# Kernel tuning notes

Hardware: AMD Instinct MI355X
Metric: run time of the kernel (lower is better)

Reference implementation:

```python
import jax, jax.numpy as jnp
import numpy as np

B, S, D, H = 1, 2048, 1024, 16
HD = D // H
S_SLOPE = 10.0      # soft_thres_layer s
C_MASK = -10000.0   # soft_thres_layer c == masked_bias
ALPHA = 0.0         # config.threshold
W_STD = 0.02        # GPT2 init std for weights


def setup_inputs() -> dict:
    key = jax.random.key(0)
    k1, k2, k3 = jax.random.split(key, 3)
    return {
        "hidden_states": jax.random.normal(k1, (B, S, D), dtype=jnp.float32),
        "c_attn_w": jax.random.normal(k2, (D, 3 * D), dtype=jnp.float32) * W_STD,
        "c_attn_b": jnp.zeros((3 * D,), dtype=jnp.float32),
        "c_proj_w": jax.random.normal(k3, (D, D), dtype=jnp.float32) * W_STD,
        "c_proj_b": jnp.zeros((D,), dtype=jnp.float32),
    }


def reference(hidden_states, c_attn_w, c_attn_b, c_proj_w, c_proj_b):
    # Conv1D: x @ w + b (GPT2 convention: weight is [in, out])
    qkv = hidden_states @ c_attn_w + c_attn_b            # [B,S,3D]
    q, k, v = jnp.split(qkv, 3, axis=-1)

    def split_heads(x):
        return x.reshape(B, S, H, HD).transpose(0, 2, 1, 3)  # [B,H,S,hd]

    q, k, v = split_heads(q), split_heads(k), split_heads(v)

    # prun path: NO 1/sqrt(d) scaling (skipped when self.prun is True)
    w = jnp.einsum("bhqd,bhkd->bhqk", q, k)              # [B,H,S,S]

    causal = jnp.tril(jnp.ones((S, S), dtype=bool))[None, None]
    w = jnp.where(causal, w, C_MASK)

    # soft-threshold pruning: smoothly pushes scores below alpha toward c=-10000
    w = C_MASK + (w - C_MASK) * jax.nn.sigmoid(S_SLOPE * (w - ALPHA))

    a = jax.nn.softmax(w, axis=-1)                        # attn_dropout = identity (eval)
    out = jnp.einsum("bhqk,bhkd->bhqd", a, v)             # [B,H,S,hd]
    out = out.transpose(0, 2, 1, 3).reshape(B, S, D)      # merge heads
    return out @ c_proj_w + c_proj_b                      # resid_dropout = identity
```

## Files before the change

kernel.cpp:

```cpp
#include <hip/hip_runtime.h>


#define S_LEN 2048
#define DM    1024
#define NH    16
#define HD    64
#define SLOPE 10.0f
#define CMASK -10000.0f
#define SP    2080

typedef short s16x4 __attribute__((ext_vector_type(4)));
typedef short s16x8 __attribute__((ext_vector_type(8)));
typedef float f32x4 __attribute__((ext_vector_type(4)));

#define MFMA16(a,b,c) __builtin_amdgcn_mfma_f32_16x16x32_bf16(a,b,c,0,0,0)
#define GLDS16(g,l) __builtin_amdgcn_global_load_lds( \
    (const __attribute__((address_space(1))) void*)(g), \
    (__attribute__((address_space(3))) void*)(l), 16, 0, 0)

__device__ __forceinline__ short f2bf(float f){
    unsigned u = __float_as_uint(f);
    u += 0x7fffu + ((u >> 16) & 1u);
    return (short)(u >> 16);
}
__device__ __forceinline__ float bf2f(short x){
    return __uint_as_float(((unsigned)(unsigned short)x) << 16);
}
struct bfpair { short hi, lo; };
__device__ __forceinline__ bfpair split_bf(float x){
    bfpair r; r.hi = f2bf(x);
    r.lo = f2bf(x - bf2f(r.hi));
    return r;
}

__device__ __forceinline__ float softthr(float sv){
    float E = __expf(-SLOPE*sv);
    float w = sv - __fdividef((sv - CMASK)*E, 1.f + E);
    return (sv > -1.5f) ? w : CMASK;
}

template<int ROWS, int THREADS>
__device__ __forceinline__ void stage_tile(const short* gbase, int rstride,
                                           short* lds, int tid){
#pragma unroll
    for (int it = 0; it < ROWS*8/THREADS; ++it){
        int s = it*THREADS + tid;
        int row = s >> 3, grp = s & 7;
        const short* src = gbase + (size_t)row*rstride + ((grp ^ (row & 7)) << 3);
        GLDS16(src, lds + (size_t)s*8);
    }
}
__device__ __forceinline__ s16x8 frag(const short* lds, int row, int kg){
    return *(const s16x8*)&lds[row*64 + ((kg ^ (row & 7)) << 3)];
}

__global__ __launch_bounds__(256)
void prep(const float* __restrict__ hs, const float* __restrict__ wqkv,
          const float* __restrict__ wprj, short* __restrict__ Ahl,
          short* __restrict__ WqT, short* __restrict__ WkvT,
          short* __restrict__ WpT)
{
    __shared__ float t[64][65];
    const int bx = blockIdx.x, tid = threadIdx.x;

    if (bx < 2048){
        int i = bx*256 + tid;
        int elem = i*4, row = elem >> 10, col = elem & 1023;
        float4 v = *(const float4*)&hs[(size_t)elem];
        bfpair a = split_bf(v.x), b = split_bf(v.y), c = split_bf(v.z), d = split_bf(v.w);
        s16x4 hv, lv;
        hv.x = a.hi; hv.y = b.hi; hv.z = c.hi; hv.w = d.hi;
        lv.x = a.lo; lv.y = b.lo; lv.z = c.lo; lv.w = d.lo;
        *(s16x4*)&Ahl[(size_t)row*2048 + col] = hv;
        *(s16x4*)&Ahl[(size_t)row*2048 + 1024 + col] = lv;
        return;
    }

    const float* W; int N, u;
    if (bx < 2816){ u = bx - 2048; W = wqkv; N = 3072; }
    else          { u = bx - 2816; W = wprj; N = 1024; }
    const int ntiles = N >> 6;
    const int tn = (u % ntiles)*64, tk = (u / ntiles)*64;

#pragma unroll
    for (int it = 0; it < 4; ++it){
        int idx = tid + it*256;
        int r = idx >> 4, c4 = (idx & 15)*4;
        float4 v = *(const float4*)&W[(size_t)(tk + r)*N + tn + c4];
        t[r][c4] = v.x; t[r][c4+1] = v.y; t[r][c4+2] = v.z; t[r][c4+3] = v.w;
    }
    __syncthreads();
#pragma unroll
    for (int it = 0; it < 4; ++it){
        int idx = tid + it*256;
        int n = idx >> 4, c4 = (idx & 15)*4;
        s16x4 hv, lv;
#pragma unroll
        for (int j = 0; j < 4; ++j){
            bfpair p = split_bf(t[c4+j][n]);
            hv[j] = p.hi; lv[j] = p.lo;
        }
        if (bx >= 2816){
            *(s16x4*)&WpT[(size_t)(tn + n)*1024 + tk + c4] = hv;
        } else if (tn < 1024){
            *(s16x4*)&WqT[(size_t)(tn + n)*2048 + tk + c4] = hv;
            *(s16x4*)&WqT[(size_t)(tn + n)*2048 + 1024 + tk + c4] = lv;
        } else {
            *(s16x4*)&WkvT[(size_t)(tn + n - 1024)*1024 + tk + c4] = hv;
        }
    }
}

__global__ __launch_bounds__(256)
void gemm_qkv(const short* __restrict__ Ahl, const short* __restrict__ WqT,
              const short* __restrict__ WkvT, const float* __restrict__ bias,
              short* __restrict__ QHh, short* __restrict__ QHl,
              short* __restrict__ KH,  short* __restrict__ Vb)
{
    __shared__ __align__(16) short Ah_s[128*64];
    __shared__ __align__(16) short Bh_s[128*64];

    const int tid = threadIdx.x, lane = tid & 63, wid = tid >> 6;
    const int lr = lane & 15, lg = lane >> 4;
    const int brow = blockIdx.y*128;
    const int xs = blockIdx.x % 3, xi = blockIdx.x / 3;
    const int bcol = xs*1024 + xi*128;
    const bool isQ = (xs == 0);
    const int KTOT = isQ ? 3072 : 1024;
    const short* Bbase = isQ ? (WqT + (size_t)bcol*2048)
                             : (WkvT + (size_t)(bcol - 1024)*1024);
    const int bstride = isQ ? 2048 : 1024;
    const int wm = (wid >> 1)*64, wn = (wid & 1)*64;

    f32x4 acc[4][4];
#pragma unroll
    for (int m = 0; m < 4; ++m)
#pragma unroll
        for (int n = 0; n < 4; ++n) acc[m][n] = (f32x4){0.f,0.f,0.f,0.f};

    for (int k0 = 0; k0 < KTOT; k0 += 64){
        int acol  = (k0 < 2048) ? k0 : k0 - 2048;
        int bcolk = (isQ && k0 >= 1024) ? k0 - 1024 : k0;
        stage_tile<128,256>(Ahl + (size_t)brow*2048 + acol, 2048, Ah_s, tid);
        stage_tile<128,256>(Bbase + bcolk, bstride, Bh_s, tid);
        __syncthreads();
#pragma unroll
        for (int kc = 0; kc < 2; ++kc){
            s16x8 ah[4], bh[4];
#pragma unroll
            for (int m = 0; m < 4; ++m)
                ah[m] = frag(Ah_s, wm + m*16 + lr, kc*4 + lg);
#pragma unroll
            for (int n = 0; n < 4; ++n)
                bh[n] = frag(Bh_s, wn + n*16 + lr, kc*4 + lg);
#pragma unroll
            for (int m = 0; m < 4; ++m)
#pragma unroll
                for (int n = 0; n < 4; ++n)
                    acc[m][n] = MFMA16(ah[m], bh[n], acc[m][n]);
        }
        __syncthreads();
    }

#pragma unroll
    for (int m = 0; m < 4; ++m)
#pragma unroll
        for (int n = 0; n < 4; ++n){
            int row  = brow + wm + m*16 + lg*4;
            int gcol = bcol + wn + n*16 + lr;
            float bv = bias[gcol];
            int col1 = gcol & 1023;
            int h0 = col1 >> 6, d = col1 & 63;
#pragma unroll
            for (int v = 0; v < 4; ++v){
                float val = acc[m][n][v] + bv;
                if (xs == 0){
                    bfpair p = split_bf(val);
                    size_t o = ((size_t)h0*S_LEN + row + v)*HD + d;
                    QHh[o] = p.hi; QHl[o] = p.lo;
                } else if (xs == 1){
                    KH[((size_t)h0*S_LEN + row + v)*HD + d] = f2bf(val);
                } else {
                    Vb[(size_t)(row + v)*DM + col1] = f2bf(val);
                }
            }
        }
}

__global__ __launch_bounds__(256)
void gemm_proj(const short* __restrict__ Ahg, const short* __restrict__ Bhg,
               const float* __restrict__ bias, float* __restrict__ C)
{
    __shared__ __align__(16) short Ah_s[128*64];
    __shared__ __align__(16) short Bh_s[128*64];

    const int tid = threadIdx.x, lane = tid & 63, wid = tid >> 6;
    const int lr = lane & 15, lg = lane >> 4;
    const int brow = blockIdx.y*128, bcol = blockIdx.x*128;
    const int wm = (wid >> 1)*64, wn = (wid & 1)*64;

    f32x4 acc[4][4];
#pragma unroll
    for (int m = 0; m < 4; ++m)
#pragma unroll
        for (int n = 0; n < 4; ++n) acc[m][n] = (f32x4){0.f,0.f,0.f,0.f};

    for (int k0 = 0; k0 < DM; k0 += 64){
        stage_tile<128,256>(Ahg + (size_t)brow*DM + k0, DM, Ah_s, tid);
        stage_tile<128,256>(Bhg + (size_t)bcol*DM + k0, DM, Bh_s, tid);
        __syncthreads();
#pragma unroll
        for (int kc = 0; kc < 2; ++kc){
            s16x8 ah[4], bh[4];
#pragma unroll
            for (int m = 0; m < 4; ++m)
                ah[m] = frag(Ah_s, wm + m*16 + lr, kc*4 + lg);
#pragma unroll
            for (int n = 0; n < 4; ++n)
                bh[n] = frag(Bh_s, wn + n*16 + lr, kc*4 + lg);
#pragma unroll
            for (int m = 0; m < 4; ++m)
#pragma unroll
                for (int n = 0; n < 4; ++n)
                    acc[m][n] = MFMA16(ah[m], bh[n], acc[m][n]);
        }
        __syncthreads();
    }

#pragma unroll
    for (int m = 0; m < 4; ++m)
#pragma unroll
        for (int n = 0; n < 4; ++n){
            int row  = brow + wm + m*16 + lg*4;
            int gcol = bcol + wn + n*16 + lr;
            float bv = bias[gcol];
#pragma unroll
            for (int v = 0; v < 4; ++v)
                C[(size_t)(row + v)*DM + gcol] = acc[m][n][v] + bv;
        }
}

__global__ __launch_bounds__(256)
void vtrans(const short* __restrict__ Vb, short* __restrict__ Vt,
            float* __restrict__ PB)
{
    __shared__ short t[64][66];
    const int tid = threadIdx.x;
    const int h = blockIdx.x, b = blockIdx.y;
    const int td = h*64, ts = b*64;
#pragma unroll
    for (int it = 0; it < 4; ++it){
        int idx = tid + it*256;
        int r = idx >> 4, c4 = (idx & 15)*4;
        s16x4 v = *(const s16x4*)&Vb[(size_t)(ts + r)*DM + td + c4];
        t[r][c4] = v.x; t[r][c4+1] = v.y; t[r][c4+2] = v.z; t[r][c4+3] = v.w;
    }
    __syncthreads();
#pragma unroll
    for (int it = 0; it < 4; ++it){
        int idx = tid + it*256;
        int n = idx >> 4, c4 = (idx & 15)*4;
        s16x4 o;
#pragma unroll
        for (int j = 0; j < 4; ++j) o[j] = t[c4+j][n];
        *(s16x4*)&Vt[(size_t)(td + n)*SP + ts + c4] = o;
    }
    if (tid < 64){
        float s = 0.f;
#pragma unroll 8
        for (int r = 0; r < 64; ++r) s += bf2f(t[r][tid]);
        PB[((size_t)h*32 + b)*64 + tid] = s;
    }
}

__global__ __launch_bounds__(64)
void sv_suffix(const float* __restrict__ PB, float* __restrict__ SSV)
{
    int h = blockIdx.x, d = threadIdx.x;
    float s = 0.f;
    SSV[((size_t)h*33 + 32)*64 + d] = 0.f;
    for (int b = 31; b >= 0; --b){
        s += PB[((size_t)h*32 + b)*64 + d];
        SSV[((size_t)h*33 + b)*64 + d] = s;
    }
}

__global__ __launch_bounds__(256)
void attn_fwd(const short* __restrict__ QHh, const short* __restrict__ QHl,
              const short* __restrict__ KH, const short* __restrict__ Vt,
              short* __restrict__ acc0, short* __restrict__ acc1,
              short* __restrict__ acc2, float* __restrict__ ML)
{
    __shared__ __align__(16) short kh_s[64*64];
    __shared__ __align__(16) short vt_s[64*64];
    __shared__ __align__(16) short Ps[4][16*72];

    const int j = blockIdx.x;
    const int h = (j & 7) + 8*((j >> 3) & 1);
    const int t = j >> 4;
    int qst, c;
    if (t < 8)      { qst = t; c = 0; }
    else if (t < 24){ int u = t - 8;  qst = 8  + (u >> 1); c = u & 1; }
    else if (t < 48){ int u = t - 24; qst = 16 + u/3;      c = u - (u/3)*3; }
    else            { int u = t - 48; qst = 24 + (u >> 2); c = u & 3; }
    const int kv0 = c*8;
    const int kv1 = min(kv0 + 8, qst + 1);

    const int tid = threadIdx.x, lane = tid & 63, wid = tid >> 6;
    const int lr = lane & 15, lg = lane >> 4;
    const int qrow = qst*64 + wid*16 + lg*4;

    const short* qbh = QHh + ((size_t)h*S_LEN + qst*64 + wid*16)*HD;
    const short* qbl = QHl + ((size_t)h*S_LEN + qst*64 + wid*16)*HD;
    s16x8 aqh[2], aql[2];
#pragma unroll
    for (int kc = 0; kc < 2; ++kc){
        aqh[kc] = *(const s16x8*)&qbh[lr*HD + kc*32 + lg*8];
        aql[kc] = *(const s16x8*)&qbl[lr*HD + kc*32 + lg*8];
    }

    float m_run[4], l_run[4];
    f32x4 acc_o[4];
#pragma unroll
    for (int v = 0; v < 4; ++v){ m_run[v] = -1e30f; l_run[v] = 0.f; }
#pragma unroll
    for (int n = 0; n < 4; ++n) acc_o[n] = (f32x4){0.f,0.f,0.f,0.f};

    for (int kvb = kv0; kvb < kv1; ++kvb){
        __syncthreads();
        stage_tile<64,256>(KH + ((size_t)h*S_LEN + kvb*64)*HD, HD, kh_s, tid);
        stage_tile<64,256>(Vt + (size_t)(h*HD)*SP + kvb*64, SP, vt_s, tid);
        __syncthreads();

        f32x4 sc[4];
#pragma unroll
        for (int n = 0; n < 4; ++n) sc[n] = (f32x4){0.f,0.f,0.f,0.f};
#pragma unroll
        for (int kc = 0; kc < 2; ++kc)
#pragma unroll
            for (int n = 0; n < 4; ++n){
                s16x8 bkh = frag(kh_s, n*16 + lr, kc*4 + lg);
                sc[n] = MFMA16(aqh[kc], bkh, sc[n]);
                sc[n] = MFMA16(aql[kc], bkh, sc[n]);
            }

        float p[4][4], tmax[4];
#pragma unroll
        for (int v = 0; v < 4; ++v) tmax[v] = -1e30f;
        if (kvb == qst){
#pragma unroll
            for (int n = 0; n < 4; ++n){
                int key = kvb*64 + n*16 + lr;
#pragma unroll
                for (int v = 0; v < 4; ++v){
                    float w = (key > qrow + v) ? CMASK : softthr(sc[n][v]);
                    p[n][v] = w;
                    tmax[v] = fmaxf(tmax[v], w);
                }
            }
        } else {
#pragma unroll
            for (int n = 0; n < 4; ++n)
#pragma unroll
                for (int v = 0; v < 4; ++v){
                    float w = softthr(sc[n][v]);
                    p[n][v] = w;
                    tmax[v] = fmaxf(tmax[v], w);
                }
        }
#pragma unroll
        for (int v = 0; v < 4; ++v)
#pragma unroll
            for (int msk = 1; msk < 16; msk <<= 1)
                tmax[v] = fmaxf(tmax[v], __shfl_xor(tmax[v], msk, 64));

        float scale[4], rsum[4];
#pragma unroll
        for (int v = 0; v < 4; ++v){
            float mn = fmaxf(m_run[v], tmax[v]);
            scale[v] = __expf(m_run[v] - mn);
            m_run[v] = mn;
            rsum[v] = 0.f;
        }
#pragma unroll
        for (int n = 0; n < 4; ++n)
#pragma unroll
            for (int v = 0; v < 4; ++v){
                float e = __expf(p[n][v] - m_run[v]);
                p[n][v] = e;
                rsum[v] += e;
            }
#pragma unroll
        for (int v = 0; v < 4; ++v){
#pragma unroll
            for (int msk = 1; msk < 16; msk <<= 1)
                rsum[v] += __shfl_xor(rsum[v], msk, 64);
            l_run[v] = l_run[v]*scale[v] + rsum[v];
        }
#pragma unroll
        for (int n = 0; n < 4; ++n)
#pragma unroll
            for (int v = 0; v < 4; ++v) acc_o[n][v] *= scale[v];

#pragma unroll
        for (int n = 0; n < 4; ++n)
#pragma unroll
            for (int v = 0; v < 4; ++v)
                Ps[wid][(lg*4 + v)*72 + 16*n + lr] = f2bf(p[n][v]);
        asm volatile("s_waitcnt lgkmcnt(0)" ::: "memory");

        s16x8 pa0 = *(const s16x8*)&Ps[wid][lr*72 + lg*8];
        s16x8 pa1 = *(const s16x8*)&Ps[wid][lr*72 + 32 + lg*8];
#pragma unroll
        for (int n = 0; n < 4; ++n){
            s16x8 bv0 = frag(vt_s, 16*n + lr, lg);
            s16x8 bv1 = frag(vt_s, 16*n + lr, 4 + lg);
            acc_o[n] = MFMA16(pa0, bv0, acc_o[n]);
            acc_o[n] = MFMA16(pa1, bv1, acc_o[n]);
        }
    }

    short* ab = (j < 512)  ? acc0 + (size_t)j*4096
              : (j < 1024) ? acc1 + (size_t)(j-512)*4096
                           : acc2 + (size_t)(j-1024)*4096;
#pragma unroll
    for (int n = 0; n < 4; ++n)
#pragma unroll
        for (int v = 0; v < 4; ++v)
            ab[(wid*16 + lg*4 + v)*64 + 16*n + lr] = f2bf(acc_o[n][v]);
    if (lr == 0){
#pragma unroll
        for (int v = 0; v < 4; ++v){
            ML[((size_t)j*64 + wid*16 + lg*4 + v)*2 + 0] = m_run[v];
            ML[((size_t)j*64 + wid*16 + lg*4 + v)*2 + 1] = l_run[v];
        }
    }
}

__global__ __launch_bounds__(256)
void attn_merge(const short* __restrict__ acc0, const short* __restrict__ acc1,
                const short* __restrict__ acc2, const float* __restrict__ ML,
                const float* __restrict__ SSV, short* __restrict__ O)
{
    const int b = blockIdx.x;
    const int h = b & 15, qst = b >> 4;
    const int d = threadIdx.x & 63, rg = threadIdx.x >> 6;
    const int C = (qst + 8) >> 3;
    const int tbase = (qst < 8)  ? qst
                    : (qst < 16) ? 8  + 2*(qst - 8)
                    : (qst < 24) ? 24 + 3*(qst - 16)
                                 : 48 + 4*(qst - 24);
    const float F = (float)(S_LEN - 64*(qst + 1));
    const float svd = SSV[((size_t)h*33 + (qst + 1))*64 + d];

    for (int i = 0; i < 16; ++i){
        int r = rg + 4*i;
        float M = -1e30f;
        for (int c = 0; c < C; ++c){
            int job = (tbase + c)*16 + h;
            M = fmaxf(M, ML[((size_t)job*64 + r)*2]);
        }
        float num = 0.f, den = 0.f;
        for (int c = 0; c < C; ++c){
            int job = (tbase + c)*16 + h;
            float m = ML[((size_t)job*64 + r)*2];
            float l = ML[((size_t)job*64 + r)*2 + 1];
            const short* ab = (job < 512)  ? acc0 + (size_t)job*4096
                            : (job < 1024) ? acc1 + (size_t)(job-512)*4096
                                           : acc2 + (size_t)(job-1024)*4096;
            float e = __expf(m - M);
            num += e * bf2f(ab[r*64 + d]);
            den += e * l;
        }
        float et = __expf(CMASK - M);
        num += et * svd;
        den += et * F;
        O[(size_t)(qst*64 + r)*DM + h*64 + d] = f2bf(num * __fdividef(1.f, den));
    }
}

extern "C" void kernel_launch(void* const* d_in, const int* in_sizes, int n_in,
                              void* d_out, int out_size, void* d_ws, size_t ws_size,
                              hipStream_t stream)
{
    (void)in_sizes; (void)n_in; (void)out_size; (void)ws_size;
    const float* hs   = (const float*)d_in[0];
    const float* wqkv = (const float*)d_in[1];
    const float* bqkv = (const float*)d_in[2];
    const float* wprj = (const float*)d_in[3];
    const float* bprj = (const float*)d_in[4];

    char* p = (char*)d_ws;
    short* Ahl  = (short*)(p + (0ull  << 20));
    short* WqT  = (short*)(p + (8ull  << 20));
    short* WkvT = (short*)(p + (12ull << 20));
    short* WpT  = (short*)(p + (16ull << 20));
    short* QHh  = (short*)(p + (18ull << 20));
    short* QHl  = (short*)(p + (22ull << 20));
    short* KH   = (short*)(p + (26ull << 20));
    short* Vbg  = (short*)(p + (30ull << 20));
    short* VT   = (short*)(p + (34ull << 20));
    float* PB   = (float*)(p + (38ull << 20) + (256ull << 10));
    float* SSV  = (float*)(p + (38ull << 20) + (512ull << 10));
    short* O    = Ahl;
    short* accA = (short*)(p + (4ull  << 20));
    short* accB = (short*)(p + (8ull  << 20));
    short* accC = (short*)(p + (12ull << 20));
    float* ML   = (float*)(p + (14ull << 20));

    prep<<<3072, 256, 0, stream>>>(hs, wqkv, wprj, Ahl, WqT, WkvT, WpT);

    gemm_qkv<<<dim3(24, 16), 256, 0, stream>>>(
        Ahl, WqT, WkvT, bqkv, QHh, QHl, KH, Vbg);

    vtrans<<<dim3(NH, S_LEN/64), 256, 0, stream>>>(Vbg, VT, PB);
    sv_suffix<<<NH, 64, 0, stream>>>(PB, SSV);

    attn_fwd<<<1280, 256, 0, stream>>>(QHh, QHl, KH, VT, accA, accB, accC, ML);
    attn_merge<<<512, 256, 0, stream>>>(accA, accB, accC, ML, SSV, O);

    gemm_proj<<<dim3(8, 16), 256, 0, stream>>>(O, WpT, bprj, (float*)d_out);
}
```

Baseline: 195.6 us.

## Restructure QKV GEMM into fused hi/lo k-loop with 32-wide tiles; inline sigmoid

After: 176.2 us. 1.11x faster.

```diff
diff --git a/kernel.cpp b/kernel.cpp
--- a/kernel.cpp
+++ b/kernel.cpp
@@ -33,12 +33,6 @@
     return r;
 }
 
-__device__ __forceinline__ float softthr(float sv){
-    float E = __expf(-SLOPE*sv);
-    float w = sv - __fdividef((sv - CMASK)*E, 1.f + E);
-    return (sv > -1.5f) ? w : CMASK;
-}
-
 template<int ROWS, int THREADS>
 __device__ __forceinline__ void stage_tile(const short* gbase, int rstride,
                                            short* lds, int tid){
@@ -52,6 +46,21 @@
 }
 __device__ __forceinline__ s16x8 frag(const short* lds, int row, int kg){
     return *(const s16x8*)&lds[row*64 + ((kg ^ (row & 7)) << 3)];
+}
+
+template<int ROWS, int THREADS>
+__device__ __forceinline__ void stage32(const short* gbase, int rstride,
+                                        short* lds, int tid){
+#pragma unroll
+    for (int it = 0; it < ROWS*4/THREADS; ++it){
+        int s = it*THREADS + tid;
+        int row = s >> 2, grp = s & 3;
+        const short* src = gbase + (size_t)row*rstride + ((grp ^ ((row >> 1) & 3)) << 3);
+        GLDS16(src, lds + (size_t)s*8);
+    }
+}
+__device__ __forceinline__ s16x8 frag32(const short* lds, int row, int kg){
+    return *(const s16x8*)&lds[row*32 + ((kg ^ ((row >> 1) & 3)) << 3)];
 }
 
 __global__ __launch_bounds__(256)
@@ -117,8 +126,7 @@
               short* __restrict__ QHh, short* __restrict__ QHl,
               short* __restrict__ KH,  short* __restrict__ Vb)
 {
-    __shared__ __align__(16) short Ah_s[128*64];
-    __shared__ __align__(16) short Bh_s[128*64];
+    __shared__ __align__(16) short LDS[4][128*32];
 
     const int tid = threadIdx.x, lane = tid & 63, wid = tid >> 6;
     const int lr = lane & 15, lg = lane >> 4;
@@ -126,10 +134,10 @@
     const int xs = blockIdx.x % 3, xi = blockIdx.x / 3;
     const int bcol = xs*1024 + xi*128;
     const bool isQ = (xs == 0);
-    const int KTOT = isQ ? 3072 : 1024;
-    const short* Bbase = isQ ? (WqT + (size_t)bcol*2048)
+    const short* Abase = Ahl + (size_t)brow*2048;
+    const short* Bbase = isQ ? (WqT + (size_t)(xi*128)*2048)
                              : (WkvT + (size_t)(bcol - 1024)*1024);
-    const int bstride = isQ ? 2048 : 1024;
+    const int bstr = isQ ? 2048 : 1024;
     const int wm = (wid >> 1)*64, wn = (wid & 1)*64;
 
     f32x4 acc[4][4];
@@ -138,27 +146,39 @@
 #pragma unroll
         for (int n = 0; n < 4; ++n) acc[m][n] = (f32x4){0.f,0.f,0.f,0.f};
 
-    for (int k0 = 0; k0 < KTOT; k0 += 64){
-        int acol  = (k0 < 2048) ? k0 : k0 - 2048;
-        int bcolk = (isQ && k0 >= 1024) ? k0 - 1024 : k0;
-        stage_tile<128,256>(Ahl + (size_t)brow*2048 + acol, 2048, Ah_s, tid);
-        stage_tile<128,256>(Bbase + bcolk, bstride, Bh_s, tid);
+    for (int k0 = 0; k0 < 1024; k0 += 32){
+        stage32<128,256>(Abase + k0, 2048, LDS[0], tid);
+        stage32<128,256>(Bbase + k0, bstr, LDS[2], tid);
+        if (isQ){
+            stage32<128,256>(Abase + 1024 + k0, 2048, LDS[1], tid);
+            stage32<128,256>(Bbase + 1024 + k0, 2048, LDS[3], tid);
+        }
         __syncthreads();
-#pragma unroll
-        for (int kc = 0; kc < 2; ++kc){
-            s16x8 ah[4], bh[4];
+        s16x8 ah[4], al[4], bh[4], bl[4];
+#pragma unroll
+        for (int m = 0; m < 4; ++m)
+            ah[m] = frag32(LDS[0], wm + m*16 + lr, lg);
+#pragma unroll
+        for (int n = 0; n < 4; ++n)
+            bh[n] = frag32(LDS[2], wn + n*16 + lr, lg);
+        if (isQ){
 #pragma unroll
             for (int m = 0; m < 4; ++m)
-                ah[m] = frag(Ah_s, wm + m*16 + lr, kc*4 + lg);
+                al[m] = frag32(LDS[1], wm + m*16 + lr, lg);
 #pragma unroll
             for (int n = 0; n < 4; ++n)
-                bh[n] = frag(Bh_s, wn + n*16 + lr, kc*4 + lg);
-#pragma unroll
-            for (int m = 0; m < 4; ++m)
-#pragma unroll
-                for (int n = 0; n < 4; ++n)
-                    acc[m][n] = MFMA16(ah[m], bh[n], acc[m][n]);
-        }
+                bl[n] = frag32(LDS[3], wn + n*16 + lr, lg);
+        }
+#pragma unroll
+        for (int m = 0; m < 4; ++m)
+#pragma unroll
+            for (int n = 0; n < 4; ++n){
+                acc[m][n] = MFMA16(ah[m], bh[n], acc[m][n]);
+                if (isQ){
+                    acc[m][n] = MFMA16(ah[m], bl[n], acc[m][n]);
+                    acc[m][n] = MFMA16(al[m], bh[n], acc[m][n]);
+                }
+            }
         __syncthreads();
     }
 
@@ -353,7 +373,13 @@
                 int key = kvb*64 + n*16 + lr;
 #pragma unroll
                 for (int v = 0; v < 4; ++v){
-                    float w = (key > qrow + v) ? CMASK : softthr(sc[n][v]);
+                    float w;
+                    if (key > qrow + v) w = CMASK;
+                    else {
+                        float sv = sc[n][v];
+                        float sig = 1.f / (1.f + __expf(-SLOPE*sv));
+                        w = CMASK + (sv - CMASK)*sig;
+                    }
                     p[n][v] = w;
                     tmax[v] = fmaxf(tmax[v], w);
                 }
@@ -363,7 +389,9 @@
             for (int n = 0; n < 4; ++n)
 #pragma unroll
                 for (int v = 0; v < 4; ++v){
-                    float w = softthr(sc[n][v]);
+                    float sv = sc[n][v];
+                    float sig = 1.f / (1.f + __expf(-SLOPE*sv));
+                    float w = CMASK + (sv - CMASK)*sig;
                     p[n][v] = w;
                     tmax[v] = fmaxf(tmax[v], w);
                 }
```
